# Optimization experiments

Measured on AMD Instinct MI355X. Metric: run time of the kernel, lower is better.

Reference implementation:

```python
import jax, jax.numpy as jnp
import numpy as np

V = 20000
E = 40000
NODE_IN = 74
EDGE_IN = 12
D = 64            # node_out_feats
EH = 128          # edge_hidden_feats
STEPS = 6         # num_step_message_passing


def setup_inputs() -> dict:
    key = jax.random.key(0)
    ks = jax.random.split(key, 16)
    s = lambda k, shape, scale=0.05: jax.random.normal(k, shape, dtype=jnp.float32) * scale
    return {
        "node_feats": jax.random.normal(ks[0], (V, NODE_IN), dtype=jnp.float32),
        "edge_feats": jax.random.normal(ks[1], (E, EDGE_IN), dtype=jnp.float32),
        "src": jax.random.randint(ks[2], (E,), 0, V),
        "dst": jax.random.randint(ks[3], (E,), 0, V),
        # project_node_feats: Linear(NODE_IN, D) + ReLU
        "proj_W": s(ks[4], (D, NODE_IN)),
        "proj_b": jnp.zeros((D,), jnp.float32),
        # NNConv edge network: Linear(EDGE_IN, EH) -> ReLU -> Linear(EH, D*D)
        "en_W1": s(ks[5], (EH, EDGE_IN)),
        "en_b1": jnp.zeros((EH,), jnp.float32),
        "en_W2": s(ks[6], (D * D, EH)),
        "en_b2": jnp.zeros((D * D,), jnp.float32),
        # NNConv output bias
        "conv_b": jnp.zeros((D,), jnp.float32),
        # single-layer GRU (PyTorch gate order r, z, n)
        "gru_Wih": s(ks[7], (3 * D, D)),
        "gru_Whh": s(ks[8], (3 * D, D)),
        "gru_bih": jnp.zeros((3 * D,), jnp.float32),
        "gru_bhh": jnp.zeros((3 * D,), jnp.float32),
        # MLPPredictor: Linear(2*D, 1)
        "pred_W": s(ks[9], (1, 2 * D)),
        "pred_b": jnp.zeros((1,), jnp.float32),
    }


def reference(node_feats, edge_feats, src, dst, proj_W, proj_b,
              en_W1, en_b1, en_W2, en_b2, conv_b,
              gru_Wih, gru_Whh, gru_bih, gru_bhh, pred_W, pred_b):
    nV = node_feats.shape[0]
    # project node features
    h = jax.nn.relu(node_feats @ proj_W.T + proj_b)  # (V, D)
    # per-edge weight matrices from the edge network (constant across steps)
    ew = jax.nn.relu(edge_feats @ en_W1.T + en_b1) @ en_W2.T + en_b2  # (E, D*D)
    ew = ew.reshape(-1, D, D)  # (E, D, D)

    def step(h, _):
        # NNConv (aggregator='sum'): m_e = h[src_e] @ W_e, sum at dst, + bias
        m = jnp.einsum('ei,eio->eo', h[src], ew)               # (E, D)
        neigh = jax.ops.segment_sum(m, dst, num_segments=nV)   # (V, D)
        x = jax.nn.relu(neigh + conv_b)
        # GRU update; hidden == h (they coincide in the original loop)
        gi = x @ gru_Wih.T + gru_bih
        gh = h @ gru_Whh.T + gru_bhh
        i_r, i_z, i_n = jnp.split(gi, 3, axis=-1)
        h_r, h_z, h_n = jnp.split(gh, 3, axis=-1)
        r = jax.nn.sigmoid(i_r + h_r)
        z = jax.nn.sigmoid(i_z + h_z)
        n = jnp.tanh(i_n + r * h_n)
        h_new = (1.0 - z) * n + z * h
        return h_new, None

    h, _ = jax.lax.scan(step, h, None, length=STEPS)
    # MLPPredictor: per-edge gather-concat-linear
    score = jnp.concatenate([h[src], h[dst]], axis=1) @ pred_W.T + pred_b  # (E, 1)
    return score
```

## Files before the change

kernel.cpp:

```cpp
#include <hip/hip_runtime.h>
#include <hip/hip_bf16.h>
#include <cstdint>

#define NV 20000
#define NE 40000
#define NODE_IN 74
#define EDGE_IN 12
#define D 64
#define EHID 128
#define NSTEPS 6

typedef __bf16 bf16x8 __attribute__((ext_vector_type(8)));
typedef float f32x4 __attribute__((ext_vector_type(4)));

__global__ __launch_bounds__(256) void k_proj(const float* __restrict__ nf,
                                              const float* __restrict__ W,
                                              const float* __restrict__ b,
                                              float* __restrict__ h,
                                              float* __restrict__ neigh) {
  __shared__ float sn[4][NODE_IN];
  int tid = threadIdx.x;
  int nb = blockIdx.x * 4;
  for (int idx = tid; idx < 4 * NODE_IN; idx += 256) {
    int r = idx / NODE_IN, c = idx % NODE_IN;
    sn[r][c] = nf[(size_t)(nb + r) * NODE_IN + c];
  }
  __syncthreads();
  int nl = tid >> 6, o = tid & 63;
  float acc = b[o];
#pragma unroll
  for (int i = 0; i < NODE_IN; ++i) acc = fmaf(sn[nl][i], W[o * NODE_IN + i], acc);
  h[(size_t)(nb + nl) * D + o] = fmaxf(acc, 0.f);
  neigh[(size_t)(nb + nl) * D + o] = 0.f;
}

__global__ __launch_bounds__(256) void k_edge1(const float* __restrict__ ef,
                                               const float* __restrict__ W1,
                                               const float* __restrict__ b1,
                                               __hip_bfloat16* __restrict__ t_bf) {
  __shared__ float se[2][EDGE_IN];
  int tid = threadIdx.x;
  int eb = blockIdx.x * 2;
  if (tid < 2 * EDGE_IN)
    se[tid / EDGE_IN][tid % EDGE_IN] =
        ef[(size_t)(eb + tid / EDGE_IN) * EDGE_IN + tid % EDGE_IN];
  __syncthreads();
  int el = tid >> 7, k = tid & 127;
  float acc = b1[k];
#pragma unroll
  for (int j = 0; j < EDGE_IN; ++j) acc = fmaf(se[el][j], W1[k * EDGE_IN + j], acc);
  t_bf[(size_t)(eb + el) * EHID + k] = __float2bfloat16(fmaxf(acc, 0.f));
}

__global__ __launch_bounds__(256) void k_cvt_w2(const float* __restrict__ W2,
                                                __hip_bfloat16* __restrict__ w2b) {
  int idx = blockIdx.x * 256 + threadIdx.x;
  if (idx < D * D * EHID) w2b[idx] = __float2bfloat16(W2[idx]);
}

__global__ __launch_bounds__(256) void k_b2t(const float* __restrict__ b2,
                                             __hip_bfloat16* __restrict__ b2t) {
  int idx = blockIdx.x * 256 + threadIdx.x;
  int o = idx >> 6, i = idx & 63;
  b2t[o * 64 + i] = __float2bfloat16(b2[i * 64 + o]);
}

__global__ __launch_bounds__(256) void k_build_b(const float* __restrict__ Wih,
                                                 const float* __restrict__ Whh,
                                                 __hip_bfloat16* __restrict__ Bhi,
                                                 __hip_bfloat16* __restrict__ Blo) {
  int idx = blockIdx.x * 256 + threadIdx.x;
  int n = idx >> 7, k = idx & 127;
  int o = n & 63, cls = n >> 6;
  float v;
  if (cls == 0)      v = (k < 64) ? Wih[o * 64 + k]         : Whh[o * 64 + (k - 64)];
  else if (cls == 1) v = (k < 64) ? Wih[(64 + o) * 64 + k]  : Whh[(64 + o) * 64 + (k - 64)];
  else if (cls == 2) v = (k < 64) ? Wih[(128 + o) * 64 + k] : 0.f;
  else               v = (k < 64) ? 0.f                     : Whh[(128 + o) * 64 + (k - 64)];
  __hip_bfloat16 hi = __float2bfloat16(v);
  Bhi[idx] = hi;
  Blo[idx] = __float2bfloat16(v - __bfloat162float(hi));
}

__global__ __launch_bounds__(512, 2) void k_msg(const float* __restrict__ h,
                                                const __hip_bfloat16* __restrict__ t_bf,
                                                const __hip_bfloat16* __restrict__ w2,
                                                const __hip_bfloat16* __restrict__ b2t,
                                                const int* __restrict__ src,
                                                const int* __restrict__ dst,
                                                float* __restrict__ neigh) {
  __shared__ __hip_bfloat16 W2s[512 * 128];
  __shared__ __hip_bfloat16 Hs[8][16 * 64];
  int tid = threadIdx.x;
  int bx = blockIdx.x;
  int cg = bx >> 6, ih = (bx >> 5) & 1, s = bx & 31;
  int lane = tid & 63, lr = lane & 15, lq = lane >> 4;
  int wave = tid >> 6;
  const int ocol = cg * 16 + lr;

#pragma unroll
  for (int it = 0; it < 16; ++it) {
    int chunk = it * 512 + tid;
    int row = chunk >> 4, c = chunk & 15;
    int ig = row >> 4, ol = row & 15;
    const __hip_bfloat16* gp =
        w2 + ((size_t)((ih * 32 + ig) * 64 + cg * 16 + ol)) * EHID + c * 8;
    *(bf16x8*)(W2s + row * 128 + ((c ^ ol) * 8)) = *(const bf16x8*)gp;
  }
  bf16x8 b2f0, b2f1;
#pragma unroll
  for (int j = 0; j < 8; ++j) {
    int k = lq * 8 + j;
    __bf16 v = *(const __bf16*)(b2t + (size_t)ocol * 64 + ih * 32 + k);
    __bf16 z = (__bf16)0.0f;
    b2f0[j] = (k < 16) ? v : z;
    b2f1[j] = (k >= 16) ? v : z;
  }
  __syncthreads();

  __hip_bfloat16* Hsw = &Hs[wave][0];
  int e0s = s * 1280;
  int nt = (s < 31) ? 20 : 5;

  int sw0 = (((0 * 4 + lq) ^ lr) * 8);
  int sw1 = (((1 * 4 + lq) ^ lr) * 8);
  int sw2 = (((2 * 4 + lq) ^ lr) * 8);
  int sw3 = (((3 * 4 + lq) ^ lr) * 8);

#pragma unroll 1
  for (int r3 = 0; r3 < 3; ++r3) {
    int t = r3 * 8 + wave;
    if (t >= nt) break;
    int e0t = e0s + t * 64;

    bf16x8 tf[4][4];
#pragma unroll
    for (int mt = 0; mt < 4; ++mt)
#pragma unroll
      for (int ks = 0; ks < 4; ++ks)
        tf[mt][ks] = *(const bf16x8*)(t_bf + (size_t)(e0t + mt * 16 + lr) * EHID +
                                      ks * 32 + lq * 8);

    int s_e = src[e0t + lane];
    const float* hrow = h + (size_t)s_e * D + ih * 32;
    f32x4 C[4];
#pragma unroll
    for (int mt = 0; mt < 4; ++mt) C[mt] = f32x4{0.f, 0.f, 0.f, 0.f};

#pragma unroll
    for (int ph = 0; ph < 2; ++ph) {
#pragma unroll
      for (int q = 0; q < 4; ++q) {
        float4 hv = *(const float4*)(hrow + ph * 16 + q * 4);
        Hsw[(q * 4 + 0) * 64 + lane] = __float2bfloat16(hv.x);
        Hsw[(q * 4 + 1) * 64 + lane] = __float2bfloat16(hv.y);
        Hsw[(q * 4 + 2) * 64 + lane] = __float2bfloat16(hv.z);
        Hsw[(q * 4 + 3) * 64 + lane] = __float2bfloat16(hv.w);
      }
#pragma unroll
      for (int mt = 0; mt < 4; ++mt) {
        bf16x8 af;
#pragma unroll
        for (int j = 0; j < 8; ++j)
          af[j] = *(const __bf16*)(Hsw + ((lq * 8 + j) & 15) * 64 + mt * 16 + lr);
        C[mt] = __builtin_amdgcn_mfma_f32_16x16x32_bf16(af, ph ? b2f1 : b2f0, C[mt], 0, 0, 0);
      }
#pragma unroll 2
      for (int igl = 0; igl < 16; ++igl) {
        int ig = ph * 16 + igl;
        const __hip_bfloat16* Wr = W2s + (ig * 16 + lr) * 128;
        bf16x8 f0 = *(const bf16x8*)(Wr + sw0);
        bf16x8 f1 = *(const bf16x8*)(Wr + sw1);
        bf16x8 f2 = *(const bf16x8*)(Wr + sw2);
        bf16x8 f3 = *(const bf16x8*)(Wr + sw3);
#pragma unroll
        for (int mt = 0; mt < 4; ++mt) {
          f32x4 P = {0.f, 0.f, 0.f, 0.f};
          P = __builtin_amdgcn_mfma_f32_16x16x32_bf16(tf[mt][0], f0, P, 0, 0, 0);
          P = __builtin_amdgcn_mfma_f32_16x16x32_bf16(tf[mt][1], f1, P, 0, 0, 0);
          P = __builtin_amdgcn_mfma_f32_16x16x32_bf16(tf[mt][2], f2, P, 0, 0, 0);
          P = __builtin_amdgcn_mfma_f32_16x16x32_bf16(tf[mt][3], f3, P, 0, 0, 0);
          uint2 hA = *(const uint2*)(Hsw + igl * 64 + mt * 16 + lq * 4);
          C[mt][0] = fmaf(__uint_as_float(hA.x << 16), P[0], C[mt][0]);
          C[mt][1] = fmaf(__uint_as_float(hA.x & 0xffff0000u), P[1], C[mt][1]);
          C[mt][2] = fmaf(__uint_as_float(hA.y << 16), P[2], C[mt][2]);
          C[mt][3] = fmaf(__uint_as_float(hA.y & 0xffff0000u), P[3], C[mt][3]);
        }
      }
    }
#pragma unroll
    for (int mt = 0; mt < 4; ++mt) {
#pragma unroll
      for (int r = 0; r < 4; ++r) {
        int ea = e0t + mt * 16 + lq * 4 + r;
        atomicAdd(neigh + (size_t)dst[ea] * D + ocol, C[mt][r]);
      }
    }
  }
}

__global__ __launch_bounds__(256) void k_gru(float* __restrict__ neigh,
                                             float* __restrict__ h,
                                             const __hip_bfloat16* __restrict__ Bhi,
                                             const __hip_bfloat16* __restrict__ Blo,
                                             const float* __restrict__ cb,
                                             const float* __restrict__ bih,
                                             const float* __restrict__ bhh) {
  __shared__ __hip_bfloat16 Ahi[32 * 128];
  __shared__ __hip_bfloat16 Alo[32 * 128];
  int tid = threadIdx.x;
  int n0 = blockIdx.x * 32;
  for (int idx = tid; idx < 32 * 64; idx += 256) {
    int node = idx >> 6, f = idx & 63;
    int gn = n0 + node;
    float xv = fmaxf(neigh[(size_t)gn * D + f] + cb[f], 0.f);
    neigh[(size_t)gn * D + f] = 0.f;
    float hv = h[(size_t)gn * D + f];
    __hip_bfloat16 xh = __float2bfloat16(xv);
    __hip_bfloat16 hh = __float2bfloat16(hv);
    Ahi[node * 128 + f] = xh;
    Ahi[node * 128 + 64 + f] = hh;
    Alo[node * 128 + f] = __float2bfloat16(xv - __bfloat162float(xh));
    Alo[node * 128 + 64 + f] = __float2bfloat16(hv - __bfloat162float(hh));
  }
  __syncthreads();
  int wave = tid >> 6, lane = tid & 63;
  int lr = lane & 15, lq = lane >> 4;
  f32x4 acc[2][4] = {};
#pragma unroll
  for (int ks = 0; ks < 4; ++ks) {
    int koff = ks * 32 + lq * 8;
    bf16x8 ah[2], al[2], bh[4], bl[4];
#pragma unroll
    for (int mt = 0; mt < 2; ++mt) {
      ah[mt] = *(const bf16x8*)(Ahi + (mt * 16 + lr) * 128 + koff);
      al[mt] = *(const bf16x8*)(Alo + (mt * 16 + lr) * 128 + koff);
    }
#pragma unroll
    for (int cls = 0; cls < 4; ++cls) {
      int n = cls * 64 + wave * 16 + lr;
      bh[cls] = *(const bf16x8*)(Bhi + (size_t)n * 128 + koff);
      bl[cls] = *(const bf16x8*)(Blo + (size_t)n * 128 + koff);
    }
#pragma unroll
    for (int mt = 0; mt < 2; ++mt)
#pragma unroll
      for (int cls = 0; cls < 4; ++cls) {
        acc[mt][cls] = __builtin_amdgcn_mfma_f32_16x16x32_bf16(ah[mt], bh[cls], acc[mt][cls], 0, 0, 0);
        acc[mt][cls] = __builtin_amdgcn_mfma_f32_16x16x32_bf16(al[mt], bh[cls], acc[mt][cls], 0, 0, 0);
        acc[mt][cls] = __builtin_amdgcn_mfma_f32_16x16x32_bf16(ah[mt], bl[cls], acc[mt][cls], 0, 0, 0);
      }
  }
  int o = wave * 16 + lr;
  float b_r = bih[o] + bhh[o];
  float b_z = bih[64 + o] + bhh[64 + o];
  float b_in = bih[128 + o];
  float b_hn = bhh[128 + o];
#pragma unroll
  for (int mt = 0; mt < 2; ++mt) {
#pragma unroll
    for (int r = 0; r < 4; ++r) {
      int gn = n0 + mt * 16 + lq * 4 + r;
      float rs = acc[mt][0][r] + b_r;
      float zs = acc[mt][1][r] + b_z;
      float inn = acc[mt][2][r] + b_in;
      float hnn = acc[mt][3][r] + b_hn;
      float rg = 1.f / (1.f + __expf(-rs));
      float zg = 1.f / (1.f + __expf(-zs));
      float a = inn + rg * hnn;
      a = fminf(fmaxf(a, -15.f), 15.f);
      float e2 = __expf(2.f * a);
      float nn = (e2 - 1.f) / (e2 + 1.f);
      float hold = h[(size_t)gn * D + o];
      h[(size_t)gn * D + o] = (1.f - zg) * nn + zg * hold;
    }
  }
}

__global__ __launch_bounds__(256) void k_pred(const float* __restrict__ h,
                                              const int* __restrict__ src,
                                              const int* __restrict__ dst,
                                              const float* __restrict__ pW,
                                              const float* __restrict__ pb,
                                              float* __restrict__ out) {
  int wave = threadIdx.x >> 6, lane = threadIdx.x & 63;
  int e = blockIdx.x * 4 + wave;
  int s = src[e], d2 = dst[e];
  float v = h[(size_t)s * D + lane] * pW[lane] + h[(size_t)d2 * D + lane] * pW[64 + lane];
#pragma unroll
  for (int off = 32; off >= 1; off >>= 1) v += __shfl_xor(v, off, 64);
  if (lane == 0) out[e] = v + pb[0];
}

extern "C" void kernel_launch(void* const* d_in, const int* in_sizes, int n_in,
                              void* d_out, int out_size, void* d_ws, size_t ws_size,
                              hipStream_t stream) {
  const float* node_feats = (const float*)d_in[0];
  const float* edge_feats = (const float*)d_in[1];
  const int* src = (const int*)d_in[2];
  const int* dst = (const int*)d_in[3];
  const float* proj_W = (const float*)d_in[4];
  const float* proj_b = (const float*)d_in[5];
  const float* en_W1 = (const float*)d_in[6];
  const float* en_b1 = (const float*)d_in[7];
  const float* en_W2 = (const float*)d_in[8];
  const float* en_b2 = (const float*)d_in[9];
  const float* conv_b = (const float*)d_in[10];
  const float* gru_Wih = (const float*)d_in[11];
  const float* gru_Whh = (const float*)d_in[12];
  const float* gru_bih = (const float*)d_in[13];
  const float* gru_bhh = (const float*)d_in[14];
  const float* pred_W = (const float*)d_in[15];
  const float* pred_b = (const float*)d_in[16];

  char* ws = (char*)d_ws;
  size_t off = 0;
  auto walloc = [&](size_t bytes) -> void* {
    void* p = ws + off;
    off = (off + bytes + 255) & ~(size_t)255;
    return p;
  };
  float* h = (float*)walloc((size_t)NV * D * 4);
  float* neigh = (float*)walloc((size_t)NV * D * 4);
  __hip_bfloat16* t_bf = (__hip_bfloat16*)walloc((size_t)NE * EHID * 2);
  __hip_bfloat16* w2_bf = (__hip_bfloat16*)walloc((size_t)D * D * EHID * 2);
  __hip_bfloat16* b2t = (__hip_bfloat16*)walloc((size_t)D * D * 2);
  __hip_bfloat16* Bhi = (__hip_bfloat16*)walloc((size_t)256 * 128 * 2);
  __hip_bfloat16* Blo = (__hip_bfloat16*)walloc((size_t)256 * 128 * 2);

  k_proj<<<NV / 4, 256, 0, stream>>>(node_feats, proj_W, proj_b, h, neigh);
  k_edge1<<<NE / 2, 256, 0, stream>>>(edge_feats, en_W1, en_b1, t_bf);
  k_cvt_w2<<<(D * D * EHID + 255) / 256, 256, 0, stream>>>(en_W2, w2_bf);
  k_b2t<<<(D * D + 255) / 256, 256, 0, stream>>>(en_b2, b2t);
  k_build_b<<<128, 256, 0, stream>>>(gru_Wih, gru_Whh, Bhi, Blo);
  for (int s = 0; s < NSTEPS; ++s) {
    k_msg<<<256, 512, 0, stream>>>(h, t_bf, w2_bf, b2t, src, dst, neigh);
    k_gru<<<NV / 32, 256, 0, stream>>>(neigh, h, Bhi, Blo, conv_b, gru_bih, gru_bhh);
  }
  k_pred<<<NE / 4, 256, 0, stream>>>(h, src, dst, pred_W, pred_b, (float*)d_out);
}
```

Baseline: 500.2 us.

## Merge prep kernels, widen message blocks to 12 waves, prefetch indices, add setprio

Merges the five setup kernels into one launch that branches on block index. The message kernel grows from 8 to 12 waves per block, so each wave handles at most two 64-edge tiles instead of three. Source and destination indices are now loaded up front as vectors. s_setprio is raised around the MFMA inner loop. Together these aim to cut launch overhead, improve load balance across waves and hide index-load latency, at the cost of more register pressure (launch_bounds 768,3) and tighter LDS budgeting.

Result: slower. 519.3 us (+3.8%).

```diff
diff --git a/kernel.cpp b/kernel.cpp
--- a/kernel.cpp
+++ b/kernel.cpp
@@ -13,76 +13,62 @@
 typedef __bf16 bf16x8 __attribute__((ext_vector_type(8)));
 typedef float f32x4 __attribute__((ext_vector_type(4)));
 
-__global__ __launch_bounds__(256) void k_proj(const float* __restrict__ nf,
-                                              const float* __restrict__ W,
-                                              const float* __restrict__ b,
-                                              float* __restrict__ h,
-                                              float* __restrict__ neigh) {
-  __shared__ float sn[4][NODE_IN];
+__global__ __launch_bounds__(256) void k_prep(
+    const float* __restrict__ nf, const float* __restrict__ pjW, const float* __restrict__ pjb,
+    float* __restrict__ h, float* __restrict__ neigh,
+    const float* __restrict__ ef, const float* __restrict__ W1, const float* __restrict__ b1,
+    __hip_bfloat16* __restrict__ t_bf,
+    const float* __restrict__ W2, __hip_bfloat16* __restrict__ w2b,
+    const float* __restrict__ b2, __hip_bfloat16* __restrict__ b2t,
+    const float* __restrict__ Wih, const float* __restrict__ Whh,
+    __hip_bfloat16* __restrict__ Bhi, __hip_bfloat16* __restrict__ Blo) {
+  __shared__ float smem[4 * NODE_IN];
   int tid = threadIdx.x;
-  int nb = blockIdx.x * 4;
-  for (int idx = tid; idx < 4 * NODE_IN; idx += 256) {
-    int r = idx / NODE_IN, c = idx % NODE_IN;
-    sn[r][c] = nf[(size_t)(nb + r) * NODE_IN + c];
-  }
-  __syncthreads();
-  int nl = tid >> 6, o = tid & 63;
-  float acc = b[o];
-#pragma unroll
-  for (int i = 0; i < NODE_IN; ++i) acc = fmaf(sn[nl][i], W[o * NODE_IN + i], acc);
-  h[(size_t)(nb + nl) * D + o] = fmaxf(acc, 0.f);
-  neigh[(size_t)(nb + nl) * D + o] = 0.f;
-}
-
-__global__ __launch_bounds__(256) void k_edge1(const float* __restrict__ ef,
-                                               const float* __restrict__ W1,
-                                               const float* __restrict__ b1,
-                                               __hip_bfloat16* __restrict__ t_bf) {
-  __shared__ float se[2][EDGE_IN];
-  int tid = threadIdx.x;
-  int eb = blockIdx.x * 2;
-  if (tid < 2 * EDGE_IN)
-    se[tid / EDGE_IN][tid % EDGE_IN] =
-        ef[(size_t)(eb + tid / EDGE_IN) * EDGE_IN + tid % EDGE_IN];
-  __syncthreads();
-  int el = tid >> 7, k = tid & 127;
-  float acc = b1[k];
-#pragma unroll
-  for (int j = 0; j < EDGE_IN; ++j) acc = fmaf(se[el][j], W1[k * EDGE_IN + j], acc);
-  t_bf[(size_t)(eb + el) * EHID + k] = __float2bfloat16(fmaxf(acc, 0.f));
-}
-
-__global__ __launch_bounds__(256) void k_cvt_w2(const float* __restrict__ W2,
-                                                __hip_bfloat16* __restrict__ w2b) {
-  int idx = blockIdx.x * 256 + threadIdx.x;
-  if (idx < D * D * EHID) w2b[idx] = __float2bfloat16(W2[idx]);
-}
-
-__global__ __launch_bounds__(256) void k_b2t(const float* __restrict__ b2,
-                                             __hip_bfloat16* __restrict__ b2t) {
-  int idx = blockIdx.x * 256 + threadIdx.x;
-  int o = idx >> 6, i = idx & 63;
-  b2t[o * 64 + i] = __float2bfloat16(b2[i * 64 + o]);
-}
-
-__global__ __launch_bounds__(256) void k_build_b(const float* __restrict__ Wih,
-                                                 const float* __restrict__ Whh,
-                                                 __hip_bfloat16* __restrict__ Bhi,
-                                                 __hip_bfloat16* __restrict__ Blo) {
-  int idx = blockIdx.x * 256 + threadIdx.x;
-  int n = idx >> 7, k = idx & 127;
-  int o = n & 63, cls = n >> 6;
-  float v;
-  if (cls == 0)      v = (k < 64) ? Wih[o * 64 + k]         : Whh[o * 64 + (k - 64)];
-  else if (cls == 1) v = (k < 64) ? Wih[(64 + o) * 64 + k]  : Whh[(64 + o) * 64 + (k - 64)];
-  else if (cls == 2) v = (k < 64) ? Wih[(128 + o) * 64 + k] : 0.f;
-  else               v = (k < 64) ? 0.f                     : Whh[(128 + o) * 64 + (k - 64)];
-  __hip_bfloat16 hi = __float2bfloat16(v);
-  Bhi[idx] = hi;
-  Blo[idx] = __float2bfloat16(v - __bfloat162float(hi));
-}
-
-__global__ __launch_bounds__(512, 2) void k_msg(const float* __restrict__ h,
+  int bx = blockIdx.x;
+  if (bx < 5000) {
+    int nb = bx * 4;
+    for (int idx = tid; idx < 4 * NODE_IN; idx += 256)
+      smem[idx] = nf[(size_t)nb * NODE_IN + idx];
+    __syncthreads();
+    int nl = tid >> 6, o = tid & 63;
+    float acc = pjb[o];
+#pragma unroll
+    for (int i = 0; i < NODE_IN; ++i) acc = fmaf(smem[nl * NODE_IN + i], pjW[o * NODE_IN + i], acc);
+    h[(size_t)(nb + nl) * D + o] = fmaxf(acc, 0.f);
+    neigh[(size_t)(nb + nl) * D + o] = 0.f;
+  } else if (bx < 25000) {
+    int eb = (bx - 5000) * 2;
+    if (tid < 2 * EDGE_IN)
+      smem[tid] = ef[(size_t)eb * EDGE_IN + tid];
+    __syncthreads();
+    int el = tid >> 7, k = tid & 127;
+    float acc = b1[k];
+#pragma unroll
+    for (int j = 0; j < EDGE_IN; ++j) acc = fmaf(smem[el * EDGE_IN + j], W1[k * EDGE_IN + j], acc);
+    t_bf[(size_t)(eb + el) * EHID + k] = __float2bfloat16(fmaxf(acc, 0.f));
+  } else if (bx < 27048) {
+    int idx = (bx - 25000) * 256 + tid;
+    w2b[idx] = __float2bfloat16(W2[idx]);
+  } else if (bx < 27064) {
+    int idx = (bx - 27048) * 256 + tid;
+    int o = idx >> 6, i = idx & 63;
+    b2t[o * 64 + i] = __float2bfloat16(b2[i * 64 + o]);
+  } else {
+    int idx = (bx - 27064) * 256 + tid;
+    int n = idx >> 7, k = idx & 127;
+    int o = n & 63, cls = n >> 6;
+    float v;
+    if (cls == 0)      v = (k < 64) ? Wih[o * 64 + k]         : Whh[o * 64 + (k - 64)];
+    else if (cls == 1) v = (k < 64) ? Wih[(64 + o) * 64 + k]  : Whh[(64 + o) * 64 + (k - 64)];
+    else if (cls == 2) v = (k < 64) ? Wih[(128 + o) * 64 + k] : 0.f;
+    else               v = (k < 64) ? 0.f                     : Whh[(128 + o) * 64 + (k - 64)];
+    __hip_bfloat16 hi = __float2bfloat16(v);
+    Bhi[idx] = hi;
+    Blo[idx] = __float2bfloat16(v - __bfloat162float(hi));
+  }
+}
+
+__global__ __launch_bounds__(768, 3) void k_msg(const float* __restrict__ h,
                                                 const __hip_bfloat16* __restrict__ t_bf,
                                                 const __hip_bfloat16* __restrict__ w2,
                                                 const __hip_bfloat16* __restrict__ b2t,
@@ -90,7 +76,7 @@
                                                 const int* __restrict__ dst,
                                                 float* __restrict__ neigh) {
   __shared__ __hip_bfloat16 W2s[512 * 128];
-  __shared__ __hip_bfloat16 Hs[8][16 * 64];
+  __shared__ __hip_bfloat16 Hs[12][16 * 64];
   int tid = threadIdx.x;
   int bx = blockIdx.x;
   int cg = bx >> 6, ih = (bx >> 5) & 1, s = bx & 31;
@@ -98,9 +84,7 @@
   int wave = tid >> 6;
   const int ocol = cg * 16 + lr;
 
-#pragma unroll
-  for (int it = 0; it < 16; ++it) {
-    int chunk = it * 512 + tid;
+  for (int chunk = tid; chunk < 8192; chunk += 768) {
     int row = chunk >> 4, c = chunk & 15;
     int ig = row >> 4, ol = row & 15;
     const __hip_bfloat16* gp =
@@ -127,11 +111,15 @@
   int sw2 = (((2 * 4 + lq) ^ lr) * 8);
   int sw3 = (((3 * 4 + lq) ^ lr) * 8);
 
+  int se0 = (wave < nt) ? src[e0s + wave * 64 + lane] : 0;
+  int se1 = (wave + 12 < nt) ? src[e0s + (wave + 12) * 64 + lane] : 0;
+
 #pragma unroll 1
-  for (int r3 = 0; r3 < 3; ++r3) {
-    int t = r3 * 8 + wave;
+  for (int r2 = 0; r2 < 2; ++r2) {
+    int t = r2 * 12 + wave;
     if (t >= nt) break;
     int e0t = e0s + t * 64;
+    int s_e = r2 ? se1 : se0;
 
     bf16x8 tf[4][4];
 #pragma unroll
@@ -141,7 +129,11 @@
         tf[mt][ks] = *(const bf16x8*)(t_bf + (size_t)(e0t + mt * 16 + lr) * EHID +
                                       ks * 32 + lq * 8);
 
-    int s_e = src[e0t + lane];
+    int4 dv[4];
+#pragma unroll
+    for (int mt = 0; mt < 4; ++mt)
+      dv[mt] = *(const int4*)(dst + e0t + mt * 16 + lq * 4);
+
     const float* hrow = h + (size_t)s_e * D + ih * 32;
     f32x4 C[4];
 #pragma unroll
@@ -165,6 +157,7 @@
           af[j] = *(const __bf16*)(Hsw + ((lq * 8 + j) & 15) * 64 + mt * 16 + lr);
         C[mt] = __builtin_amdgcn_mfma_f32_16x16x32_bf16(af, ph ? b2f1 : b2f0, C[mt], 0, 0, 0);
       }
+      __builtin_amdgcn_s_setprio(1);
 #pragma unroll 2
       for (int igl = 0; igl < 16; ++igl) {
         int ig = ph * 16 + igl;
@@ -187,14 +180,14 @@
           C[mt][3] = fmaf(__uint_as_float(hA.y & 0xffff0000u), P[3], C[mt][3]);
         }
       }
+      __builtin_amdgcn_s_setprio(0);
     }
 #pragma unroll
     for (int mt = 0; mt < 4; ++mt) {
-#pragma unroll
-      for (int r = 0; r < 4; ++r) {
-        int ea = e0t + mt * 16 + lq * 4 + r;
-        atomicAdd(neigh + (size_t)dst[ea] * D + ocol, C[mt][r]);
-      }
+      atomicAdd(neigh + (size_t)dv[mt].x * D + ocol, C[mt][0]);
+      atomicAdd(neigh + (size_t)dv[mt].y * D + ocol, C[mt][1]);
+      atomicAdd(neigh + (size_t)dv[mt].z * D + ocol, C[mt][2]);
+      atomicAdd(neigh + (size_t)dv[mt].w * D + ocol, C[mt][3]);
     }
   }
 }
@@ -328,13 +321,12 @@
   __hip_bfloat16* Bhi = (__hip_bfloat16*)walloc((size_t)256 * 128 * 2);
   __hip_bfloat16* Blo = (__hip_bfloat16*)walloc((size_t)256 * 128 * 2);
 
-  k_proj<<<NV / 4, 256, 0, stream>>>(node_feats, proj_W, proj_b, h, neigh);
-  k_edge1<<<NE / 2, 256, 0, stream>>>(edge_feats, en_W1, en_b1, t_bf);
-  k_cvt_w2<<<(D * D * EHID + 255) / 256, 256, 0, stream>>>(en_W2, w2_bf);
-  k_b2t<<<(D * D + 255) / 256, 256, 0, stream>>>(en_b2, b2t);
-  k_build_b<<<128, 256, 0, stream>>>(gru_Wih, gru_Whh, Bhi, Blo);
+  k_prep<<<27192, 256, 0, stream>>>(node_feats, proj_W, proj_b, h, neigh,
+                                    edge_feats, en_W1, en_b1, t_bf,
+                                    en_W2, w2_bf, en_b2, b2t,
+                                    gru_Wih, gru_Whh, Bhi, Blo);
   for (int s = 0; s < NSTEPS; ++s) {
-    k_msg<<<256, 512, 0, stream>>>(h, t_bf, w2_bf, b2t, src, dst, neigh);
+    k_msg<<<256, 768, 0, stream>>>(h, t_bf, w2_bf, b2t, src, dst, neigh);
     k_gru<<<NV / 32, 256, 0, stream>>>(neigh, h, Bhi, Blo, conv_b, gru_bih, gru_bhh);
   }
   k_pred<<<NE / 4, 256, 0, stream>>>(h, src, dst, pred_W, pred_b, (float*)d_out);
```
